# Kernel optimization log

Measured on AMD Instinct MI355X. Metric: run time of the kernel, lower is better.

Reference implementation:

```python
import jax, jax.numpy as jnp
import numpy as np

NS = 0.4      # neighborhood_size
GS = 8        # grid_size
RNN = 128     # rnn_size
EMB = 64      # embedding_size
NMIX = 20     # nmixtures
N = 1024      # num pedestrians


def setup_inputs() -> dict:
    key = jax.random.key(0)
    ks = jax.random.split(key, 14)
    s = 0.05
    return {
        "xoff": jax.random.normal(ks[0], (N, 2)) * s,
        "xabs": jax.random.uniform(ks[1], (N, 2)),
        "h0": jax.random.normal(ks[2], (1, N, RNN)) * 0.1,
        "c0": jax.random.normal(ks[3], (1, N, RNN)) * 0.1,
        "W_emb": jax.random.normal(ks[4], (EMB, 2)) * s,
        "b_emb": jax.random.normal(ks[5], (EMB,)) * s,
        "W_soc": jax.random.normal(ks[6], (EMB, GS * GS * RNN)) * s,
        "b_soc": jax.random.normal(ks[7], (EMB,)) * s,
        "W_ih": jax.random.normal(ks[8], (4 * RNN, 2 * EMB)) * s,
        "W_hh": jax.random.normal(ks[9], (4 * RNN, RNN)) * s,
        "b_ih": jax.random.normal(ks[10], (4 * RNN,)) * s,
        "b_hh": jax.random.normal(ks[11], (4 * RNN,)) * s,
        "W_out": jax.random.normal(ks[12], (6 * NMIX, RNN)) * s,
        "b_out": jax.random.normal(ks[13], (6 * NMIX,)) * s,
    }


def grid_mask(xabs, dtype):
    # Vectorized getGridMask: [N, N, GS*GS] one-hot neighbor binning.
    x, y = xabs[:, 0], xabs[:, 1]
    dx = x[None, :] - (x[:, None] - NS / 2)  # other_x - width_low, [N, N]
    dy = y[None, :] - (y[:, None] - NS / 2)
    cx = jnp.floor(dx / NS * GS).astype(jnp.int32)
    cy = jnp.floor(dy / NS * GS).astype(jnp.int32)
    n = x.shape[0]
    valid = ((dx >= 0) & (dx < NS) & (dy >= 0) & (dy < NS)
             & (cx >= 0) & (cx < GS) & (cy >= 0) & (cy < GS)
             & ~jnp.eye(n, dtype=bool))
    cell = jnp.clip(cx + cy * GS, 0, GS * GS - 1)
    return jax.nn.one_hot(cell, GS * GS, dtype=dtype) * valid[..., None].astype(dtype)


def reference(xoff, xabs, h0, c0, W_emb, b_emb, W_soc, b_soc,
              W_ih, W_hh, b_ih, b_hh, W_out, b_out):
    n = xabs.shape[0]
    # predict_distance=True -> embed offsets
    emb = jax.nn.relu(xoff @ W_emb.T + b_emb)                 # [N, 64]
    grid = grid_mask(xabs, emb.dtype)                          # [N, N, 64]
    h = h0[0]                                                  # [N, 128]
    # getSocialTensor: scatter neighbor hidden states into grid bins
    social = jnp.einsum('nmg,mh->ngh', grid, h).reshape(n, GS * GS * RNN)
    pool = jax.nn.relu(social @ W_soc.T + b_soc)               # [N, 64]
    xin = jnp.concatenate([emb, pool], axis=-1)                # [N, 128]
    # single-step LSTM, torch gate order i, f, g, o
    gates = xin @ W_ih.T + h @ W_hh.T + b_ih + b_hh            # [N, 512]
    i, f, g, o = jnp.split(gates, 4, axis=-1)
    c = jax.nn.sigmoid(f) * c0[0] + jax.nn.sigmoid(i) * jnp.tanh(g)
    hn = jax.nn.sigmoid(o) * jnp.tanh(c)
    out = hn @ W_out.T + b_out                                 # [N, 120]
    mu1, mu2, ls1, ls2, rho, pi_logits = jnp.split(out, 6, axis=1)
    return (mu1, mu2, ls1, ls2, rho, pi_logits)
```

## Files before the change

### kernel.cpp

```cpp
#include <hip/hip_runtime.h>
#include <hip/hip_bf16.h>

#define NN_ 1024

#define U_WIHT 0
#define U_WHHT 65536
#define U_WOUT 131072
#define U_P    147456

typedef __attribute__((ext_vector_type(8))) short short8;
typedef __attribute__((ext_vector_type(4))) float floatx4;

__device__ __forceinline__ float b2f_(unsigned short u) {
    return __uint_as_float(((unsigned)u) << 16);
}
__device__ __forceinline__ unsigned short f2bu(float f) {
    __hip_bfloat16 b = __float2bfloat16(f);
    return *(unsigned short*)&b;
}
__device__ __forceinline__ float ldin(const void* p, int i, int isbf) {
    return isbf ? b2f_(((const unsigned short*)p)[i]) : ((const float*)p)[i];
}
__device__ __forceinline__ int detect_bf16(const void* Wih, int tid) {
    unsigned wv = ((const unsigned*)Wih)[tid];
    unsigned e8 = (wv >> 7) & 0xFFu;
    return (__syncthreads_count((e8 >= 96u && e8 <= 134u) ? 1 : 0) > 128) ? 1 : 0;
}
__device__ __forceinline__ void split8f(const float* p, short8& hi, short8& lo) {
    const float4 f0 = *(const float4*)p;
    const float4 f1 = *(const float4*)(p + 4);
    float x[8] = {f0.x, f0.y, f0.z, f0.w, f1.x, f1.y, f1.z, f1.w};
    unsigned short* H = (unsigned short*)&hi;
    unsigned short* L = (unsigned short*)&lo;
#pragma unroll
    for (int i = 0; i < 8; i++) {
        unsigned short h = f2bu(x[i]);
        H[i] = h;
        L[i] = f2bu(x[i] - b2f_(h));
    }
}

__global__ __launch_bounds__(256) void pgemm_kernel(const void* __restrict__ Wsoc,
                                                    const void* __restrict__ h0,
                                                    const void* __restrict__ Wih,
                                                    const void* __restrict__ Whh,
                                                    const void* __restrict__ Wout,
                                                    float* __restrict__ ws) {
    const int tid = threadIdx.x;
    const int isbf = detect_bf16(Wih, tid);
    unsigned short* u16w = (unsigned short*)ws;
    unsigned short* P16  = u16w + U_P;
    const int lane = tid & 63;
    const int wv   = tid >> 6;
    const int B    = blockIdx.y * 64 + blockIdx.x;
    const int mtile = B & 63;
    const int cg    = B >> 6;
    const int m = lane & 15;
    const int q = lane >> 4;
    const int abase = (mtile * 16 + m) * 128 + q * 8;
    short8 ah[4], al[4];
    if (isbf) {
        const unsigned short* H = (const unsigned short*)h0;
#pragma unroll
        for (int j = 0; j < 4; j++) {
            ah[j] = *(const short8*)(H + abase + 32 * j);
            al[j] = short8{0, 0, 0, 0, 0, 0, 0, 0};
        }
    } else {
        const float* H = (const float*)h0;
#pragma unroll
        for (int j = 0; j < 4; j++) split8f(H + abase + 32 * j, ah[j], al[j]);
    }
    const int rowl = mtile * 16 + q * 4;
#pragma unroll
    for (int t = 0; t < 4; t++) {
        const int n0 = cg * 256 + wv * 64 + t * 16;
        const int nc = n0 + m;
        const int e = nc & 63, g = nc >> 6;
        const int wb = e * 8192 + g * 128 + q * 8;
        short8 bh[4], bl[4];
        if (isbf) {
            const unsigned short* W = (const unsigned short*)Wsoc;
#pragma unroll
            for (int j = 0; j < 4; j++) {
                bh[j] = *(const short8*)(W + wb + 32 * j);
                bl[j] = short8{0, 0, 0, 0, 0, 0, 0, 0};
            }
        } else {
            const float* W = (const float*)Wsoc;
#pragma unroll
            for (int j = 0; j < 4; j++) split8f(W + wb + 32 * j, bh[j], bl[j]);
        }
        floatx4 c = {0.0f, 0.0f, 0.0f, 0.0f};
#pragma unroll
        for (int j = 0; j < 4; j++) c = __builtin_amdgcn_mfma_f32_16x16x32_bf16(ah[j], bh[j], c, 0, 0, 0);
#pragma unroll
        for (int j = 0; j < 4; j++) c = __builtin_amdgcn_mfma_f32_16x16x32_bf16(ah[j], bl[j], c, 0, 0, 0);
#pragma unroll
        for (int j = 0; j < 4; j++) c = __builtin_amdgcn_mfma_f32_16x16x32_bf16(al[j], bh[j], c, 0, 0, 0);
#pragma unroll
        for (int r = 0; r < 4; r++)
            P16[(rowl + r) * 4096 + n0 + m] = f2bu(c[r]);
    }
    if (B < 144) {
        int base = B * 1024;
        for (int i = tid; i < 1024; i += 256) {
            int t = base + i;
            float v;
            if (t < 65536)       { int k = t >> 9, j = t & 511;       v = ldin(Wih, j * 128 + k, isbf); }
            else if (t < 131072) { int t2 = t - 65536; int k = t2 >> 9, j = t2 & 511; v = ldin(Whh, j * 128 + k, isbf); }
            else                 { int t2 = t - 131072; int r = t2 >> 7, j = t2 & 127;
                                   v = (j < 120) ? ldin(Wout, j * 128 + r, isbf) : 0.0f; }
            u16w[t] = f2bu(v);
        }
    }
}

__global__ __launch_bounds__(256) void pool_lstm_kernel(
        const void* __restrict__ xoff, const void* __restrict__ xabs,
        const void* __restrict__ h0,   const void* __restrict__ c0,
        const void* __restrict__ W_emb, const void* __restrict__ b_emb,
        const void* __restrict__ b_soc, const void* __restrict__ b_ih,
        const void* __restrict__ b_hh,  const void* __restrict__ b_out,
        const void* __restrict__ Wih_det,
        const float* __restrict__ ws, float* __restrict__ out) {
    __shared__ float xabs_s[2048];
    __shared__ int   off[2][NN_];
    __shared__ int   cnt_s[2];
    __shared__ float4 red4[2][8][16];
    __shared__ __align__(16) float xin[2][128];
    __shared__ __align__(16) float hs[2][128];
    __shared__ __align__(16) float gl[2][512];
    __shared__ __align__(16) float hnl[2][128];
    const int tid = threadIdx.x;
    const int isbf = detect_bf16(Wih_det, tid);
    const int n0 = blockIdx.x * 2;
    const unsigned short* u16 = (const unsigned short*)ws;

    for (int i = tid; i < 2048; i += 256) xabs_s[i] = ldin(xabs, i, isbf);
    if (tid < 2) cnt_s[tid] = 0;
    __syncthreads();

    const int half = tid >> 7;
    const int t2 = tid & 127;
    const int n = n0 + half;
    {
        float xs = xabs_s[2 * n]     - 0.2f;
        float ys = xabs_s[2 * n + 1] - 0.2f;
        for (int i = t2; i < NN_; i += 128) {
            float dx = xabs_s[2 * i]     - xs;
            float dy = xabs_s[2 * i + 1] - ys;
            int cx = (int)floorf(dx / 0.4f * 8.0f);
            int cy = (int)floorf(dy / 0.4f * 8.0f);
            bool valid = (dx >= 0.0f) && (dx < 0.4f) && (dy >= 0.0f) && (dy < 0.4f)
                      && (cx >= 0) && (cx < 8) && (cy >= 0) && (cy < 8) && (i != n);
            if (valid) {
                int idx = atomicAdd(&cnt_s[half], 1);
                off[half][idx] = i * 4096 + ((cy * 8 + cx) << 6);
            }
        }
    }
    __syncthreads();
    {
        const unsigned short* P16 = (const unsigned short*)ws + U_P;
        const int strm = t2 >> 4, e4 = t2 & 15;
        const int cc = cnt_s[half];
        float ax = 0.0f, ay = 0.0f, az = 0.0f, aw = 0.0f;
        for (int j = strm; j < cc; j += 8) {
            int o = off[half][j];
            ushort4 u = *(const ushort4*)(P16 + o + 4 * e4);
            ax += b2f_(u.x); ay += b2f_(u.y); az += b2f_(u.z); aw += b2f_(u.w);
        }
        red4[half][strm][e4] = make_float4(ax, ay, az, aw);
    }
    __syncthreads();
    if (t2 < 16) {
        float4 s = make_float4(0.0f, 0.0f, 0.0f, 0.0f);
#pragma unroll
        for (int s8 = 0; s8 < 8; s8++) {
            float4 r = red4[half][s8][t2];
            s.x += r.x; s.y += r.y; s.z += r.z; s.w += r.w;
        }
        int e = 4 * t2;
        xin[half][64 + e]     = fmaxf(s.x + ldin(b_soc, e,     isbf), 0.0f);
        xin[half][64 + e + 1] = fmaxf(s.y + ldin(b_soc, e + 1, isbf), 0.0f);
        xin[half][64 + e + 2] = fmaxf(s.z + ldin(b_soc, e + 2, isbf), 0.0f);
        xin[half][64 + e + 3] = fmaxf(s.w + ldin(b_soc, e + 3, isbf), 0.0f);
    }
    if (t2 < 64) {
        int e = t2;
        float v = fmaf(ldin(xoff, 2 * n, isbf),     ldin(W_emb, 2 * e, isbf),
                  fmaf(ldin(xoff, 2 * n + 1, isbf), ldin(W_emb, 2 * e + 1, isbf),
                       ldin(b_emb, e, isbf)));
        xin[half][e] = fmaxf(v, 0.0f);
    }
    hs[half][t2] = ldin(h0, n * 128 + t2, isbf);
    __syncthreads();
    {
        const int j0 = 2 * tid, j1 = 2 * tid + 1;
        float ax[2] = {0, 0}, ay[2] = {0, 0};
        for (int k = 0; k < 128; k += 4) {
            union { float4 v; float f[4]; } xu[2], hu[2];
#pragma unroll
            for (int nn = 0; nn < 2; nn++) {
                xu[nn].v = *(const float4*)&xin[nn][k];
                hu[nn].v = *(const float4*)&hs[nn][k];
            }
#pragma unroll
            for (int kk = 0; kk < 4; kk++) {
                ushort2 wi = *(const ushort2*)(u16 + U_WIHT + (k + kk) * 512 + j0);
                ushort2 wh = *(const ushort2*)(u16 + U_WHHT + (k + kk) * 512 + j0);
                float wix = b2f_(wi.x), wiy = b2f_(wi.y);
                float whx = b2f_(wh.x), why = b2f_(wh.y);
#pragma unroll
                for (int nn = 0; nn < 2; nn++) {
                    float xk = xu[nn].f[kk], hk = hu[nn].f[kk];
                    ax[nn] = fmaf(xk, wix, ax[nn]); ax[nn] = fmaf(hk, whx, ax[nn]);
                    ay[nn] = fmaf(xk, wiy, ay[nn]); ay[nn] = fmaf(hk, why, ay[nn]);
                }
            }
        }
        float bb0 = ldin(b_ih, j0, isbf) + ldin(b_hh, j0, isbf);
        float bb1 = ldin(b_ih, j1, isbf) + ldin(b_hh, j1, isbf);
#pragma unroll
        for (int nn = 0; nn < 2; nn++) {
            gl[nn][j0] = ax[nn] + bb0;
            gl[nn][j1] = ay[nn] + bb1;
        }
    }
    __syncthreads();
    {
        int r = t2;
        float iv = gl[half][r], fv = gl[half][r + 128];
        float gv = gl[half][r + 256], ov = gl[half][r + 384];
        float si = 1.0f / (1.0f + expf(-iv));
        float sf = 1.0f / (1.0f + expf(-fv));
        float so = 1.0f / (1.0f + expf(-ov));
        float cc = sf * ldin(c0, n * 128 + r, isbf) + si * tanhf(gv);
        hnl[half][r] = so * tanhf(cc);
    }
    __syncthreads();
    {
        int j = t2;
        if (j < 120) {
            float acc = ldin(b_out, j, isbf);
            for (int r = 0; r < 128; r += 4) {
                float4 hq = *(const float4*)&hnl[half][r];
                acc = fmaf(hq.x, b2f_(u16[U_WOUT + (r + 0) * 128 + j]), acc);
                acc = fmaf(hq.y, b2f_(u16[U_WOUT + (r + 1) * 128 + j]), acc);
                acc = fmaf(hq.z, b2f_(u16[U_WOUT + (r + 2) * 128 + j]), acc);
                acc = fmaf(hq.w, b2f_(u16[U_WOUT + (r + 3) * 128 + j]), acc);
            }
            int ch = j / 20, wc = j - ch * 20;
            out[ch * 20480 + n * 20 + wc] = acc;
        }
    }
}

extern "C" void kernel_launch(void* const* d_in, const int* in_sizes, int n_in,
                              void* d_out, int out_size, void* d_ws, size_t ws_size,
                              hipStream_t stream) {
    const void* xoff  = d_in[0];
    const void* xabs  = d_in[1];
    const void* h0    = d_in[2];
    const void* c0    = d_in[3];
    const void* W_emb = d_in[4];
    const void* b_emb = d_in[5];
    const void* W_soc = d_in[6];
    const void* b_soc = d_in[7];
    const void* W_ih  = d_in[8];
    const void* W_hh  = d_in[9];
    const void* b_ih  = d_in[10];
    const void* b_hh  = d_in[11];
    const void* W_out = d_in[12];
    const void* b_out = d_in[13];
    float* ws = (float*)d_ws;
    float* out = (float*)d_out;

    pgemm_kernel<<<dim3(64, 16), 256, 0, stream>>>(W_soc, h0, W_ih, W_hh, W_out, ws);
    pool_lstm_kernel<<<512, 256, 0, stream>>>(xoff, xabs, h0, c0, W_emb, b_emb,
                                              b_soc, b_ih, b_hh, b_out, W_ih, ws, out);
}
```

Before: 132.7 us.

## Split pipeline into prep, pgemm, pool, and MFMA-based LSTM kernels

Adds a prep kernel that converts W_soc, h0 and the embedding into bf16 hi/lo split buffers and packs W_ih and W_hh into one gate weight matrix. pgemm then only loads the pre-split data, and the pooling kernel writes its pooled features into the activation buffer. A new LSTM kernel computes the gate GEMM with bf16 MFMA over 16-row tiles instead of scalar FMAs repeated per pair of pedestrians. This trades fewer redundant weight reads and less scalar work for two extra kernel launches and extra workspace traffic.

```diff
diff --git a/kernel.cpp b/kernel.cpp
--- a/kernel.cpp
+++ b/kernel.cpp
@@ -3,10 +3,13 @@
 
 #define NN_ 1024
 
-#define U_WIHT 0
-#define U_WHHT 65536
+#define U_WG   0
 #define U_WOUT 131072
-#define U_P    147456
+#define U_SHI  147456
+#define U_SLO  671744
+#define U_ACTH 1196032
+#define U_ACTL 1458176
+#define U_P    1720320
 
 typedef __attribute__((ext_vector_type(8))) short short8;
 typedef __attribute__((ext_vector_type(4))) float floatx4;
@@ -26,70 +29,80 @@
     unsigned e8 = (wv >> 7) & 0xFFu;
     return (__syncthreads_count((e8 >= 96u && e8 <= 134u) ? 1 : 0) > 128) ? 1 : 0;
 }
-__device__ __forceinline__ void split8f(const float* p, short8& hi, short8& lo) {
-    const float4 f0 = *(const float4*)p;
-    const float4 f1 = *(const float4*)(p + 4);
-    float x[8] = {f0.x, f0.y, f0.z, f0.w, f1.x, f1.y, f1.z, f1.w};
-    unsigned short* H = (unsigned short*)&hi;
-    unsigned short* L = (unsigned short*)&lo;
-#pragma unroll
-    for (int i = 0; i < 8; i++) {
-        unsigned short h = f2bu(x[i]);
-        H[i] = h;
-        L[i] = f2bu(x[i] - b2f_(h));
-    }
-}
-
-__global__ __launch_bounds__(256) void pgemm_kernel(const void* __restrict__ Wsoc,
-                                                    const void* __restrict__ h0,
-                                                    const void* __restrict__ Wih,
-                                                    const void* __restrict__ Whh,
-                                                    const void* __restrict__ Wout,
-                                                    float* __restrict__ ws) {
+
+__global__ __launch_bounds__(256) void prep_kernel(
+        const void* __restrict__ xoff, const void* __restrict__ h0,
+        const void* __restrict__ Wsoc, const void* __restrict__ Wemb,
+        const void* __restrict__ bemb, const void* __restrict__ Wih,
+        const void* __restrict__ Whh,  const void* __restrict__ Wout,
+        float* __restrict__ ws) {
     const int tid = threadIdx.x;
     const int isbf = detect_bf16(Wih, tid);
-    unsigned short* u16w = (unsigned short*)ws;
-    unsigned short* P16  = u16w + U_P;
-    const int lane = tid & 63;
-    const int wv   = tid >> 6;
-    const int B    = blockIdx.y * 64 + blockIdx.x;
-    const int mtile = B & 63;
-    const int cg    = B >> 6;
-    const int m = lane & 15;
-    const int q = lane >> 4;
-    const int abase = (mtile * 16 + m) * 128 + q * 8;
+    unsigned short* u = (unsigned short*)ws;
+    for (int t = blockIdx.x * 256 + tid; t < 868352; t += 262144) {
+        if (t < 131072) {
+            int j = t >> 8, k = t & 255;
+            float v = (k < 128) ? ldin(Wih, j * 128 + k, isbf)
+                                : ldin(Whh, j * 128 + (k - 128), isbf);
+            u[U_WG + t] = f2bu(v);
+        } else if (t < 147456) {
+            int t2 = t - 131072; int r = t2 >> 7, j = t2 & 127;
+            u[U_WOUT + t2] = f2bu((j < 120) ? ldin(Wout, j * 128 + r, isbf) : 0.0f);
+        } else if (t < 671744) {
+            int t2 = t - 147456;
+            float x = ldin(Wsoc, t2, isbf);
+            unsigned short hi = f2bu(x);
+            u[U_SHI + t2] = hi;
+            u[U_SLO + t2] = f2bu(x - b2f_(hi));
+        } else if (t < 802816) {
+            int t2 = t - 671744; int n = t2 >> 7, k = t2 & 127;
+            float x = ldin(h0, t2, isbf);
+            unsigned short hi = f2bu(x);
+            u[U_ACTH + n * 256 + 128 + k] = hi;
+            u[U_ACTL + n * 256 + 128 + k] = f2bu(x - b2f_(hi));
+        } else {
+            int t2 = t - 802816; int n = t2 >> 6, e = t2 & 63;
+            float v = fmaf(ldin(xoff, 2 * n, isbf),     ldin(Wemb, 2 * e, isbf),
+                      fmaf(ldin(xoff, 2 * n + 1, isbf), ldin(Wemb, 2 * e + 1, isbf),
+                           ldin(bemb, e, isbf)));
+            v = fmaxf(v, 0.0f);
+            unsigned short hi = f2bu(v);
+            u[U_ACTH + n * 256 + e] = hi;
+            u[U_ACTL + n * 256 + e] = f2bu(v - b2f_(hi));
+        }
+    }
+}
+
+__global__ __launch_bounds__(256) void pgemm_kernel(float* __restrict__ ws) {
+    const unsigned short* u = (const unsigned short*)ws;
+    const short* Ah  = (const short*)(u + U_ACTH);
+    const short* Al  = (const short*)(u + U_ACTL);
+    const short* Shi = (const short*)(u + U_SHI);
+    const short* Slo = (const short*)(u + U_SLO);
+    unsigned short* P16 = (unsigned short*)ws + U_P;
+    const int tid = threadIdx.x, lane = tid & 63, wv = tid >> 6;
+    const int B_ = blockIdx.y * 64 + blockIdx.x;
+    const int mtile = B_ & 63, cgi = B_ >> 6;
+    const int m = lane & 15, q = lane >> 4;
+    const int abase = (mtile * 16 + m) * 256 + 128 + q * 8;
     short8 ah[4], al[4];
-    if (isbf) {
-        const unsigned short* H = (const unsigned short*)h0;
-#pragma unroll
-        for (int j = 0; j < 4; j++) {
-            ah[j] = *(const short8*)(H + abase + 32 * j);
-            al[j] = short8{0, 0, 0, 0, 0, 0, 0, 0};
-        }
-    } else {
-        const float* H = (const float*)h0;
-#pragma unroll
-        for (int j = 0; j < 4; j++) split8f(H + abase + 32 * j, ah[j], al[j]);
+#pragma unroll
+    for (int j = 0; j < 4; j++) {
+        ah[j] = *(const short8*)(Ah + abase + 32 * j);
+        al[j] = *(const short8*)(Al + abase + 32 * j);
     }
     const int rowl = mtile * 16 + q * 4;
 #pragma unroll
     for (int t = 0; t < 4; t++) {
-        const int n0 = cg * 256 + wv * 64 + t * 16;
+        const int n0 = cgi * 256 + wv * 64 + t * 16;
         const int nc = n0 + m;
         const int e = nc & 63, g = nc >> 6;
         const int wb = e * 8192 + g * 128 + q * 8;
         short8 bh[4], bl[4];
-        if (isbf) {
-            const unsigned short* W = (const unsigned short*)Wsoc;
-#pragma unroll
-            for (int j = 0; j < 4; j++) {
-                bh[j] = *(const short8*)(W + wb + 32 * j);
-                bl[j] = short8{0, 0, 0, 0, 0, 0, 0, 0};
-            }
-        } else {
-            const float* W = (const float*)Wsoc;
-#pragma unroll
-            for (int j = 0; j < 4; j++) split8f(W + wb + 32 * j, bh[j], bl[j]);
+#pragma unroll
+        for (int j = 0; j < 4; j++) {
+            bh[j] = *(const short8*)(Shi + wb + 32 * j);
+            bl[j] = *(const short8*)(Slo + wb + 32 * j);
         }
         floatx4 c = {0.0f, 0.0f, 0.0f, 0.0f};
 #pragma unroll
@@ -102,40 +115,20 @@
         for (int r = 0; r < 4; r++)
             P16[(rowl + r) * 4096 + n0 + m] = f2bu(c[r]);
     }
-    if (B < 144) {
-        int base = B * 1024;
-        for (int i = tid; i < 1024; i += 256) {
-            int t = base + i;
-            float v;
-            if (t < 65536)       { int k = t >> 9, j = t & 511;       v = ldin(Wih, j * 128 + k, isbf); }
-            else if (t < 131072) { int t2 = t - 65536; int k = t2 >> 9, j = t2 & 511; v = ldin(Whh, j * 128 + k, isbf); }
-            else                 { int t2 = t - 131072; int r = t2 >> 7, j = t2 & 127;
-                                   v = (j < 120) ? ldin(Wout, j * 128 + r, isbf) : 0.0f; }
-            u16w[t] = f2bu(v);
-        }
-    }
-}
-
-__global__ __launch_bounds__(256) void pool_lstm_kernel(
-        const void* __restrict__ xoff, const void* __restrict__ xabs,
-        const void* __restrict__ h0,   const void* __restrict__ c0,
-        const void* __restrict__ W_emb, const void* __restrict__ b_emb,
-        const void* __restrict__ b_soc, const void* __restrict__ b_ih,
-        const void* __restrict__ b_hh,  const void* __restrict__ b_out,
-        const void* __restrict__ Wih_det,
-        const float* __restrict__ ws, float* __restrict__ out) {
+}
+
+__global__ __launch_bounds__(256) void pool_kernel(const void* __restrict__ xabs,
+                                                   const void* __restrict__ b_soc,
+                                                   const void* __restrict__ Wih_det,
+                                                   float* __restrict__ ws) {
     __shared__ float xabs_s[2048];
     __shared__ int   off[2][NN_];
     __shared__ int   cnt_s[2];
     __shared__ float4 red4[2][8][16];
-    __shared__ __align__(16) float xin[2][128];
-    __shared__ __align__(16) float hs[2][128];
-    __shared__ __align__(16) float gl[2][512];
-    __shared__ __align__(16) float hnl[2][128];
     const int tid = threadIdx.x;
     const int isbf = detect_bf16(Wih_det, tid);
     const int n0 = blockIdx.x * 2;
-    const unsigned short* u16 = (const unsigned short*)ws;
+    unsigned short* u = (unsigned short*)ws;
 
     for (int i = tid; i < 2048; i += 256) xabs_s[i] = ldin(xabs, i, isbf);
     if (tid < 2) cnt_s[tid] = 0;
@@ -168,91 +161,95 @@
         float ax = 0.0f, ay = 0.0f, az = 0.0f, aw = 0.0f;
         for (int j = strm; j < cc; j += 8) {
             int o = off[half][j];
-            ushort4 u = *(const ushort4*)(P16 + o + 4 * e4);
-            ax += b2f_(u.x); ay += b2f_(u.y); az += b2f_(u.z); aw += b2f_(u.w);
+            ushort4 uu = *(const ushort4*)(P16 + o + 4 * e4);
+            ax += b2f_(uu.x); ay += b2f_(uu.y); az += b2f_(uu.z); aw += b2f_(uu.w);
         }
         red4[half][strm][e4] = make_float4(ax, ay, az, aw);
     }
     __syncthreads();
     if (t2 < 16) {
-        float4 s = make_float4(0.0f, 0.0f, 0.0f, 0.0f);
+        float s[4] = {0.0f, 0.0f, 0.0f, 0.0f};
 #pragma unroll
         for (int s8 = 0; s8 < 8; s8++) {
             float4 r = red4[half][s8][t2];
-            s.x += r.x; s.y += r.y; s.z += r.z; s.w += r.w;
+            s[0] += r.x; s[1] += r.y; s[2] += r.z; s[3] += r.w;
         }
         int e = 4 * t2;
-        xin[half][64 + e]     = fmaxf(s.x + ldin(b_soc, e,     isbf), 0.0f);
-        xin[half][64 + e + 1] = fmaxf(s.y + ldin(b_soc, e + 1, isbf), 0.0f);
-        xin[half][64 + e + 2] = fmaxf(s.z + ldin(b_soc, e + 2, isbf), 0.0f);
-        xin[half][64 + e + 3] = fmaxf(s.w + ldin(b_soc, e + 3, isbf), 0.0f);
-    }
-    if (t2 < 64) {
-        int e = t2;
-        float v = fmaf(ldin(xoff, 2 * n, isbf),     ldin(W_emb, 2 * e, isbf),
-                  fmaf(ldin(xoff, 2 * n + 1, isbf), ldin(W_emb, 2 * e + 1, isbf),
-                       ldin(b_emb, e, isbf)));
-        xin[half][e] = fmaxf(v, 0.0f);
-    }
-    hs[half][t2] = ldin(h0, n * 128 + t2, isbf);
-    __syncthreads();
-    {
-        const int j0 = 2 * tid, j1 = 2 * tid + 1;
-        float ax[2] = {0, 0}, ay[2] = {0, 0};
-        for (int k = 0; k < 128; k += 4) {
-            union { float4 v; float f[4]; } xu[2], hu[2];
-#pragma unroll
-            for (int nn = 0; nn < 2; nn++) {
-                xu[nn].v = *(const float4*)&xin[nn][k];
-                hu[nn].v = *(const float4*)&hs[nn][k];
-            }
-#pragma unroll
-            for (int kk = 0; kk < 4; kk++) {
-                ushort2 wi = *(const ushort2*)(u16 + U_WIHT + (k + kk) * 512 + j0);
-                ushort2 wh = *(const ushort2*)(u16 + U_WHHT + (k + kk) * 512 + j0);
-                float wix = b2f_(wi.x), wiy = b2f_(wi.y);
-                float whx = b2f_(wh.x), why = b2f_(wh.y);
-#pragma unroll
-                for (int nn = 0; nn < 2; nn++) {
-                    float xk = xu[nn].f[kk], hk = hu[nn].f[kk];
-                    ax[nn] = fmaf(xk, wix, ax[nn]); ax[nn] = fmaf(hk, whx, ax[nn]);
-                    ay[nn] = fmaf(xk, wiy, ay[nn]); ay[nn] = fmaf(hk, why, ay[nn]);
-                }
-            }
-        }
-        float bb0 = ldin(b_ih, j0, isbf) + ldin(b_hh, j0, isbf);
-        float bb1 = ldin(b_ih, j1, isbf) + ldin(b_hh, j1, isbf);
-#pragma unroll
-        for (int nn = 0; nn < 2; nn++) {
-            gl[nn][j0] = ax[nn] + bb0;
-            gl[nn][j1] = ay[nn] + bb1;
-        }
-    }
-    __syncthreads();
-    {
-        int r = t2;
-        float iv = gl[half][r], fv = gl[half][r + 128];
-        float gv = gl[half][r + 256], ov = gl[half][r + 384];
+#pragma unroll
+        for (int i = 0; i < 4; i++) {
+            float v = fmaxf(s[i] + ldin(b_soc, e + i, isbf), 0.0f);
+            unsigned short hi = f2bu(v);
+            u[U_ACTH + n * 256 + 64 + e + i] = hi;
+            u[U_ACTL + n * 256 + 64 + e + i] = f2bu(v - b2f_(hi));
+        }
+    }
+}
+
+__global__ __launch_bounds__(256) void lstm_kernel(const void* __restrict__ c0,
+                                                   const void* __restrict__ b_ih,
+                                                   const void* __restrict__ b_hh,
+                                                   const void* __restrict__ b_out,
+                                                   const void* __restrict__ Wih_det,
+                                                   float* __restrict__ ws,
+                                                   float* __restrict__ out) {
+    __shared__ float gl[16 * 516];
+    __shared__ __align__(16) float hnl[16][128];
+    const int tid = threadIdx.x;
+    const int isbf = detect_bf16(Wih_det, tid);
+    const unsigned short* u = (const unsigned short*)ws;
+    const short* Ah = (const short*)(u + U_ACTH);
+    const short* Al = (const short*)(u + U_ACTL);
+    const short* Wg = (const short*)(u + U_WG);
+    const int lane = tid & 63, wv = tid >> 6, m = lane & 15, q = lane >> 4;
+    const int m0 = blockIdx.x * 16;
+    floatx4 acc[8];
+#pragma unroll
+    for (int t = 0; t < 8; t++) acc[t] = floatx4{0.0f, 0.0f, 0.0f, 0.0f};
+    for (int ks = 0; ks < 8; ks++) {
+        const int ab = (m0 + m) * 256 + ks * 32 + q * 8;
+        short8 ah = *(const short8*)(Ah + ab);
+        short8 al = *(const short8*)(Al + ab);
+#pragma unroll
+        for (int t = 0; t < 8; t++) {
+            const int j = (wv * 8 + t) * 16 + m;
+            short8 b = *(const short8*)(Wg + j * 256 + ks * 32 + q * 8);
+            acc[t] = __builtin_amdgcn_mfma_f32_16x16x32_bf16(ah, b, acc[t], 0, 0, 0);
+            acc[t] = __builtin_amdgcn_mfma_f32_16x16x32_bf16(al, b, acc[t], 0, 0, 0);
+        }
+    }
+#pragma unroll
+    for (int t = 0; t < 8; t++) {
+        const int jc = (wv * 8 + t) * 16 + m;
+        float bias = ldin(b_ih, jc, isbf) + ldin(b_hh, jc, isbf);
+#pragma unroll
+        for (int r = 0; r < 4; r++)
+            gl[(q * 4 + r) * 516 + jc] = acc[t][r] + bias;
+    }
+    __syncthreads();
+    for (int i = tid; i < 2048; i += 256) {
+        int a = i >> 7, r = i & 127;
+        float iv = gl[a * 516 + r],       fv = gl[a * 516 + r + 128];
+        float gv = gl[a * 516 + r + 256], ov = gl[a * 516 + r + 384];
         float si = 1.0f / (1.0f + expf(-iv));
         float sf = 1.0f / (1.0f + expf(-fv));
         float so = 1.0f / (1.0f + expf(-ov));
-        float cc = sf * ldin(c0, n * 128 + r, isbf) + si * tanhf(gv);
-        hnl[half][r] = so * tanhf(cc);
-    }
-    __syncthreads();
-    {
-        int j = t2;
+        float cc = sf * ldin(c0, (m0 + a) * 128 + r, isbf) + si * tanhf(gv);
+        hnl[a][r] = so * tanhf(cc);
+    }
+    __syncthreads();
+    for (int i = tid; i < 2048; i += 256) {
+        int a = i >> 7, j = i & 127;
         if (j < 120) {
-            float acc = ldin(b_out, j, isbf);
+            float acc2 = ldin(b_out, j, isbf);
             for (int r = 0; r < 128; r += 4) {
-                float4 hq = *(const float4*)&hnl[half][r];
-                acc = fmaf(hq.x, b2f_(u16[U_WOUT + (r + 0) * 128 + j]), acc);
-                acc = fmaf(hq.y, b2f_(u16[U_WOUT + (r + 1) * 128 + j]), acc);
-                acc = fmaf(hq.z, b2f_(u16[U_WOUT + (r + 2) * 128 + j]), acc);
-                acc = fmaf(hq.w, b2f_(u16[U_WOUT + (r + 3) * 128 + j]), acc);
+                float4 hq = *(const float4*)&hnl[a][r];
+                acc2 = fmaf(hq.x, b2f_(u[U_WOUT + (r + 0) * 128 + j]), acc2);
+                acc2 = fmaf(hq.y, b2f_(u[U_WOUT + (r + 1) * 128 + j]), acc2);
+                acc2 = fmaf(hq.z, b2f_(u[U_WOUT + (r + 2) * 128 + j]), acc2);
+                acc2 = fmaf(hq.w, b2f_(u[U_WOUT + (r + 3) * 128 + j]), acc2);
             }
             int ch = j / 20, wc = j - ch * 20;
-            out[ch * 20480 + n * 20 + wc] = acc;
+            out[ch * 20480 + (m0 + a) * 20 + wc] = acc2;
         }
     }
 }
@@ -277,7 +274,9 @@
     float* ws = (float*)d_ws;
     float* out = (float*)d_out;
 
-    pgemm_kernel<<<dim3(64, 16), 256, 0, stream>>>(W_soc, h0, W_ih, W_hh, W_out, ws);
-    pool_lstm_kernel<<<512, 256, 0, stream>>>(xoff, xabs, h0, c0, W_emb, b_emb,
-                                              b_soc, b_ih, b_hh, b_out, W_ih, ws, out);
-}
+    prep_kernel<<<1024, 256, 0, stream>>>(xoff, h0, W_soc, W_emb, b_emb,
+                                          W_ih, W_hh, W_out, ws);
+    pgemm_kernel<<<dim3(64, 16), 256, 0, stream>>>(ws);
+    pool_kernel<<<512, 256, 0, stream>>>(xabs, b_soc, W_ih, ws);
+    lstm_kernel<<<64, 256, 0, stream>>>(c0, b_ih, b_hh, b_out, W_ih, ws, out);
+}
```

Measured after the change: 240.4 us. 1.81x slower.

## Pre-split W_soc and h0 into bf16 hi/lo in a prep kernel with MFMA-friendly layout

Applied to the files above, without the earlier changes.

Adds a separate prep kernel that converts W_soc and h0 into bf16 hi/lo pairs once, storing W_soc in a fragment-ordered layout so the GEMM kernel loads contiguous short8 vectors. Previously each of the 1024 GEMM blocks redid the fp32 split on strided W_soc reads, and h0 was split again by every column group. The weight transpose work also moves into the prep kernel. The cost is an extra kernel launch plus writing and re-reading about 2.6M extra bf16 values through the workspace.

```diff
diff --git a/kernel.cpp b/kernel.cpp
--- a/kernel.cpp
+++ b/kernel.cpp
@@ -6,7 +6,11 @@
 #define U_WIHT 0
 #define U_WHHT 65536
 #define U_WOUT 131072
-#define U_P    147456
+#define U_SHI  147456
+#define U_SLO  671744
+#define U_HHI  1196032
+#define U_HLO  1327104
+#define U_P    1458176
 
 typedef __attribute__((ext_vector_type(8))) short short8;
 typedef __attribute__((ext_vector_type(4))) float floatx4;
@@ -26,93 +30,82 @@
     unsigned e8 = (wv >> 7) & 0xFFu;
     return (__syncthreads_count((e8 >= 96u && e8 <= 134u) ? 1 : 0) > 128) ? 1 : 0;
 }
-__device__ __forceinline__ void split8f(const float* p, short8& hi, short8& lo) {
-    const float4 f0 = *(const float4*)p;
-    const float4 f1 = *(const float4*)(p + 4);
-    float x[8] = {f0.x, f0.y, f0.z, f0.w, f1.x, f1.y, f1.z, f1.w};
-    unsigned short* H = (unsigned short*)&hi;
-    unsigned short* L = (unsigned short*)&lo;
-#pragma unroll
-    for (int i = 0; i < 8; i++) {
-        unsigned short h = f2bu(x[i]);
-        H[i] = h;
-        L[i] = f2bu(x[i] - b2f_(h));
-    }
-}
-
-__global__ __launch_bounds__(256) void pgemm_kernel(const void* __restrict__ Wsoc,
-                                                    const void* __restrict__ h0,
-                                                    const void* __restrict__ Wih,
-                                                    const void* __restrict__ Whh,
-                                                    const void* __restrict__ Wout,
-                                                    float* __restrict__ ws) {
+
+__global__ __launch_bounds__(256) void prep_kernel(
+        const void* __restrict__ h0,  const void* __restrict__ Wsoc,
+        const void* __restrict__ Wih, const void* __restrict__ Whh,
+        const void* __restrict__ Wout, float* __restrict__ ws) {
     const int tid = threadIdx.x;
     const int isbf = detect_bf16(Wih, tid);
-    unsigned short* u16w = (unsigned short*)ws;
-    unsigned short* P16  = u16w + U_P;
-    const int lane = tid & 63;
-    const int wv   = tid >> 6;
-    const int B    = blockIdx.y * 64 + blockIdx.x;
-    const int mtile = B & 63;
-    const int cg    = B >> 6;
-    const int m = lane & 15;
-    const int q = lane >> 4;
+    unsigned short* u = (unsigned short*)ws;
+    int t = blockIdx.x * 256 + tid;
+    if (t < 65536) {
+        int k = t >> 9, j = t & 511;
+        u[U_WIHT + t] = f2bu(ldin(Wih, j * 128 + k, isbf));
+    } else if (t < 131072) {
+        int t2 = t - 65536; int k = t2 >> 9, j = t2 & 511;
+        u[U_WHHT + t2] = f2bu(ldin(Whh, j * 128 + k, isbf));
+    } else if (t < 147456) {
+        int t2 = t - 131072; int r = t2 >> 7, j = t2 & 127;
+        u[U_WOUT + t2] = f2bu((j < 120) ? ldin(Wout, j * 128 + r, isbf) : 0.0f);
+    } else if (t < 671744) {
+        int t2 = t - 147456;
+        int r = t2 & 7, e = (t2 >> 3) & 63, q = (t2 >> 9) & 3;
+        int j = (t2 >> 11) & 3, g = t2 >> 13;
+        float x = ldin(Wsoc, e * 8192 + g * 128 + j * 32 + q * 8 + r, isbf);
+        unsigned short hi = f2bu(x);
+        u[U_SHI + t2] = hi;
+        u[U_SLO + t2] = f2bu(x - b2f_(hi));
+    } else {
+        int t2 = t - 671744;
+        float x = ldin(h0, t2, isbf);
+        unsigned short hi = f2bu(x);
+        u[U_HHI + t2] = hi;
+        u[U_HLO + t2] = f2bu(x - b2f_(hi));
+    }
+}
+
+__global__ __launch_bounds__(256) void pgemm_kernel(float* __restrict__ ws) {
+    const unsigned short* u = (const unsigned short*)ws;
+    const short* Hhi = (const short*)(u + U_HHI);
+    const short* Hlo = (const short*)(u + U_HLO);
+    const short* Shi = (const short*)(u + U_SHI);
+    const short* Slo = (const short*)(u + U_SLO);
+    unsigned short* P16 = (unsigned short*)ws + U_P;
+    const int tid = threadIdx.x, lane = tid & 63, wv = tid >> 6;
+    const int B_ = blockIdx.y * 64 + blockIdx.x;
+    const int mtile = B_ & 63, cg = B_ >> 6;
+    const int m = lane & 15, q = lane >> 4;
+    const int g = cg * 4 + wv;
     const int abase = (mtile * 16 + m) * 128 + q * 8;
     short8 ah[4], al[4];
-    if (isbf) {
-        const unsigned short* H = (const unsigned short*)h0;
+#pragma unroll
+    for (int j = 0; j < 4; j++) {
+        ah[j] = *(const short8*)(Hhi + abase + 32 * j);
+        al[j] = *(const short8*)(Hlo + abase + 32 * j);
+    }
+    const int rowl = mtile * 16 + q * 4;
+#pragma unroll
+    for (int t = 0; t < 4; t++) {
+        const int e = t * 16 + m;
+        short8 bh[4], bl[4];
 #pragma unroll
         for (int j = 0; j < 4; j++) {
-            ah[j] = *(const short8*)(H + abase + 32 * j);
-            al[j] = short8{0, 0, 0, 0, 0, 0, 0, 0};
-        }
-    } else {
-        const float* H = (const float*)h0;
-#pragma unroll
-        for (int j = 0; j < 4; j++) split8f(H + abase + 32 * j, ah[j], al[j]);
-    }
-    const int rowl = mtile * 16 + q * 4;
-#pragma unroll
-    for (int t = 0; t < 4; t++) {
+            const int fb = ((g * 4 + j) * 4 + q) * 512 + e * 8;
+            bh[j] = *(const short8*)(Shi + fb);
+            bl[j] = *(const short8*)(Slo + fb);
+        }
+        floatx4 c = {0.0f, 0.0f, 0.0f, 0.0f};
+#pragma unroll
+        for (int j = 0; j < 4; j++) c = __builtin_amdgcn_mfma_f32_16x16x32_bf16(ah[j], bh[j], c, 0, 0, 0);
+#pragma unroll
+        for (int j = 0; j < 4; j++) c = __builtin_amdgcn_mfma_f32_16x16x32_bf16(ah[j], bl[j], c, 0, 0, 0);
+#pragma unroll
+        for (int j = 0; j < 4; j++) c = __builtin_amdgcn_mfma_f32_16x16x32_bf16(al[j], bh[j], c, 0, 0, 0);
         const int n0 = cg * 256 + wv * 64 + t * 16;
-        const int nc = n0 + m;
-        const int e = nc & 63, g = nc >> 6;
-        const int wb = e * 8192 + g * 128 + q * 8;
-        short8 bh[4], bl[4];
-        if (isbf) {
-            const unsigned short* W = (const unsigned short*)Wsoc;
-#pragma unroll
-            for (int j = 0; j < 4; j++) {
-                bh[j] = *(const short8*)(W + wb + 32 * j);
-                bl[j] = short8{0, 0, 0, 0, 0, 0, 0, 0};
-            }
-        } else {
-            const float* W = (const float*)Wsoc;
-#pragma unroll
-            for (int j = 0; j < 4; j++) split8f(W + wb + 32 * j, bh[j], bl[j]);
-        }
-        floatx4 c = {0.0f, 0.0f, 0.0f, 0.0f};
-#pragma unroll
-        for (int j = 0; j < 4; j++) c = __builtin_amdgcn_mfma_f32_16x16x32_bf16(ah[j], bh[j], c, 0, 0, 0);
-#pragma unroll
-        for (int j = 0; j < 4; j++) c = __builtin_amdgcn_mfma_f32_16x16x32_bf16(ah[j], bl[j], c, 0, 0, 0);
-#pragma unroll
-        for (int j = 0; j < 4; j++) c = __builtin_amdgcn_mfma_f32_16x16x32_bf16(al[j], bh[j], c, 0, 0, 0);
 #pragma unroll
         for (int r = 0; r < 4; r++)
             P16[(rowl + r) * 4096 + n0 + m] = f2bu(c[r]);
-    }
-    if (B < 144) {
-        int base = B * 1024;
-        for (int i = tid; i < 1024; i += 256) {
-            int t = base + i;
-            float v;
-            if (t < 65536)       { int k = t >> 9, j = t & 511;       v = ldin(Wih, j * 128 + k, isbf); }
-            else if (t < 131072) { int t2 = t - 65536; int k = t2 >> 9, j = t2 & 511; v = ldin(Whh, j * 128 + k, isbf); }
-            else                 { int t2 = t - 131072; int r = t2 >> 7, j = t2 & 127;
-                                   v = (j < 120) ? ldin(Wout, j * 128 + r, isbf) : 0.0f; }
-            u16w[t] = f2bu(v);
-        }
     }
 }
 
@@ -168,8 +161,8 @@
         float ax = 0.0f, ay = 0.0f, az = 0.0f, aw = 0.0f;
         for (int j = strm; j < cc; j += 8) {
             int o = off[half][j];
-            ushort4 u = *(const ushort4*)(P16 + o + 4 * e4);
-            ax += b2f_(u.x); ay += b2f_(u.y); az += b2f_(u.z); aw += b2f_(u.w);
+            ushort4 uu = *(const ushort4*)(P16 + o + 4 * e4);
+            ax += b2f_(uu.x); ay += b2f_(uu.y); az += b2f_(uu.z); aw += b2f_(uu.w);
         }
         red4[half][strm][e4] = make_float4(ax, ay, az, aw);
     }
@@ -277,7 +270,8 @@
     float* ws = (float*)d_ws;
     float* out = (float*)d_out;
 
-    pgemm_kernel<<<dim3(64, 16), 256, 0, stream>>>(W_soc, h0, W_ih, W_hh, W_out, ws);
+    prep_kernel<<<3136, 256, 0, stream>>>(h0, W_soc, W_ih, W_hh, W_out, ws);
+    pgemm_kernel<<<dim3(64, 16), 256, 0, stream>>>(ws);
     pool_lstm_kernel<<<512, 256, 0, stream>>>(xoff, xabs, h0, c0, W_emb, b_emb,
                                               b_soc, b_ih, b_hh, b_out, W_ih, ws, out);
 }
```

After: 125.8 us. 5.2% less time.
